# Kernel optimization log

Measured on AMD Instinct MI355X. Metric: run time of the kernel, lower is better.

## Reference

```python
import jax, jax.numpy as jnp
import numpy as np

K = 16        # num_p
SIGMA = 1.0
B, NA, NB, C = 2, 16384, 8192, 128
Z, Y, X = 64, 256, 256  # spatial_shape


def _unique_coords(rng, n):
    lin = rng.choice(Z * Y * X, size=n, replace=False)
    z = lin // (Y * X)
    y = (lin // X) % Y
    x = lin % X
    return np.stack([z, y, x], axis=-1).astype(np.float32)


def setup_inputs() -> dict:
    key = jax.random.key(0)
    k1, = jax.random.split(key, 1)
    rng = np.random.default_rng(0)
    # teacher voxel coords unique per batch -> bev_out_3d dedup is identity
    tpos = np.stack([_unique_coords(rng, NA) for _ in range(B)])          # [B, NA, 3]
    spos = np.stack([_unique_coords(rng, NB) for _ in range(B)])          # [B, NB, 3]
    tfeat = jax.random.normal(k1, (B, NA, C), dtype=jnp.float32)
    return {
        "teacher_features": tfeat,
        "teacher_positions": jnp.asarray(tpos),
        "student_positions": jnp.asarray(spos),
    }


def _knn_agg(feats, pa, pb):
    # feats: [NA, C], pa: [NA, 3] teacher coords, pb: [NB, 3] student coords
    # squared euclidean distances (same top-k ordering as cdist p=2)
    sq = (jnp.sum(pb * pb, -1, keepdims=True)
          - 2.0 * pb @ pa.T
          + jnp.sum(pa * pa, -1)[None, :])                                # [NB, NA]
    neg_sq_k, idx = jax.lax.top_k(-sq, K)                                 # smallest-k
    knn_sq = jnp.maximum(-neg_sq_k, 0.0)                                  # [NB, K] = knn_dist**2
    w = jnp.exp(-knn_sq / (2.0 * SIGMA ** 2))
    w = w / jnp.sum(w, axis=1, keepdims=True)
    knn_feats = feats[idx]                                                # [NB, K, C]
    return jnp.einsum('nkc,nk->nc', knn_feats, w)                         # [NB, C]


def reference(teacher_features, teacher_positions, student_positions):
    # per-batch knn_aggregation, batches have equal sizes -> vmap
    return jax.vmap(_knn_agg)(teacher_features, teacher_positions, student_positions)
```

## Files before the change

kernel.cpp:

```cpp
#include <hip/hip_runtime.h>
#include <math.h>
#include <stdint.h>

#define K_NN   16
#define BATCH  2
#define NA_    16384
#define NB_    8192
#define CH     128
#define CZ     4
#define CY     16
#define CX     16
#define NCELL  (CZ*CY*CX)
#define CSH    4
#define PADKEY 0xFFF00000u

#define OFF_META   65536
#define OFF_CURSOR 81920
#define OFF_SORTED 98304

__device__ __forceinline__ int cell_of(float p0, float p1, float p2) {
    const int cz = ((int)p0) >> CSH;
    const int cy = ((int)p1) >> CSH;
    const int cx = ((int)p2) >> CSH;
    return (cz * CY + cy) * CX + cx;
}


__global__ __launch_bounds__(256) void count_hist(const float* __restrict__ tpos,
                                                  int* __restrict__ partial) {
    __shared__ int h[NCELL];
    const int blk = blockIdx.x;
    const int t = threadIdx.x;
#pragma unroll
    for (int j = 0; j < NCELL / 256; ++j) h[t + j * 256] = 0;
    __syncthreads();
    const int base = blk * 2048;
#pragma unroll
    for (int i = 0; i < 8; ++i) {
        const float* p = tpos + (size_t)(base + i * 256 + t) * 3;
        atomicAdd(&h[cell_of(p[0], p[1], p[2])], 1);
    }
    __syncthreads();
#pragma unroll
    for (int j = 0; j < NCELL / 256; ++j) {
        const int c = t + j * 256;
        partial[blk * NCELL + c] = h[c];
    }
}


__global__ __launch_bounds__(1024) void scan_kernel(const int* __restrict__ partial,
                                                    int2* __restrict__ meta,
                                                    int* __restrict__ cursor) {
    __shared__ int wp[16];
    const int b = blockIdx.x, t = threadIdx.x, lane = t & 63, w = t >> 6;
    int c = 0;
#pragma unroll
    for (int k = 0; k < 8; ++k) c += partial[(b * 8 + k) * NCELL + t];
    int x = c;
#pragma unroll
    for (int off = 1; off < 64; off <<= 1) {
        int u = __shfl_up(x, off);
        if (lane >= off) x += u;
    }
    if (lane == 63) wp[w] = x;
    __syncthreads();
    if (t < 16) {
        int v = wp[t];
#pragma unroll
        for (int off = 1; off < 16; off <<= 1) {
            int u = __shfl_up(v, off);
            if (t >= off) v += u;
        }
        wp[t] = v;
    }
    __syncthreads();
    const int excl = x - c + (w ? wp[w - 1] : 0);
    meta[b * NCELL + t]   = make_int2(excl, c);
    cursor[b * NCELL + t] = excl;
}


__global__ __launch_bounds__(256) void scatter_kernel(const float* __restrict__ tpos,
                                                      int* __restrict__ cursor,
                                                      uint2* __restrict__ sorted) {
    const int i = blockIdx.x * 256 + threadIdx.x;
    const int b = i >> 14;
    const float* tp = tpos + (size_t)i * 3;
    const int pz = (int)tp[0], py = (int)tp[1], px = (int)tp[2];
    const int cell = ((pz >> CSH) * CY + (py >> CSH)) * CX + (px >> CSH);
    const int pos = atomicAdd(&cursor[b * NCELL + cell], 1);
    const uint32_t pk = ((uint32_t)pz << 16) | ((uint32_t)py << 8) | (uint32_t)px;
    sorted[(size_t)b * NA_ + pos] = make_uint2(pk, (uint32_t)(i & (NA_ - 1)));
}


template<int NS>
__device__ __forceinline__ void merge_extract(uint32_t (&k)[NS], uint32_t (&sel)[K_NN]) {
    uint32_t m = k[0];
#pragma unroll
    for (int j = 1; j < NS; ++j) m = min(m, k[j]);
#pragma unroll
    for (int r = 0; r < K_NN; ++r) {
        uint32_t v = m;
#pragma unroll
        for (int off = 32; off > 0; off >>= 1)
            v = min(v, (uint32_t)__shfl_xor((int)v, off));
        sel[r] = (uint32_t)__builtin_amdgcn_readfirstlane((int)v);
        if (m == v) {
#pragma unroll
            for (int j = 0; j < NS; ++j) k[j] = (k[j] == v) ? 0xFFFFFFFFu : k[j];
            m = k[0];
#pragma unroll
            for (int j = 1; j < NS; ++j) m = min(m, k[j]);
        }
    }
}

__device__ __forceinline__ uint32_t key_of(uint2 p, int sz, int sy, int sx) {
    const int pz = (int)(p.x >> 16);
    const int py = (int)((p.x >> 8) & 255u);
    const int px = (int)(p.x & 255u);
    const int dz = sz - pz, dy = sy - py, dx = sx - px;
    const uint32_t d2 = (uint32_t)(dz * dz + dy * dy + dx * dx);
    return (d2 << 14) | p.y;
}


__device__ __noinline__ void ring_fallback(int lane, int sz, int sy, int sx,
                                           int scz, int scy, int scx, int rcov,
                                           const int2* __restrict__ mb,
                                           const uint2* __restrict__ sb,
                                           uint32_t* selLds) {
    uint32_t sel[K_NN];
#pragma unroll
    for (int j = 0; j < K_NN; ++j) sel[j] = 0xFFFFFFFFu;

    for (int r = 1;; ++r) {
        uint32_t kl[K_NN];
#pragma unroll
        for (int j = 0; j < K_NN; ++j) kl[j] = PADKEY + 16 + j;
        if (r > 1) {
            uint32_t seed = 0xFFFFFFFFu;
#pragma unroll
            for (int j = 0; j < K_NN; ++j) if (lane == j) seed = sel[j];
            kl[0] = seed;
        }
        uint32_t curmax = kl[0];
#pragma unroll
        for (int j = 1; j < K_NN; ++j) curmax = max(curmax, kl[j]);

        for (int dz = -r; dz <= r; ++dz) {
            const int cz = scz + dz; if ((unsigned)cz >= CZ) continue;
            for (int dy = -r; dy <= r; ++dy) {
                const int cy = scy + dy; if ((unsigned)cy >= CY) continue;
                const int rowb = (cz * CY + cy) * CX;
                const bool fullrow = (r == 1) || (max(abs(dz), abs(dy)) == r);
                int xl[2], xh[2];
                if (fullrow) {
                    xl[0] = max(scx - r, 0); xh[0] = min(scx + r, CX - 1);
                    xl[1] = 1; xh[1] = 0;
                } else {
                    xl[0] = scx - r; xh[0] = scx - r;
                    xl[1] = scx + r; xh[1] = scx + r;
                    if (xl[0] < 0)      { xl[0] = 1; xh[0] = 0; }
                    if (xh[1] > CX - 1) { xl[1] = 1; xh[1] = 0; }
                }
#pragma unroll
                for (int q = 0; q < 2; ++q) {
                    if (xl[q] > xh[q]) continue;
                    const int2 mlo = mb[rowb + xl[q]];
                    const int2 mhi = mb[rowb + xh[q]];
                    const int st = mlo.x, ln = mhi.x + mhi.y - st;
                    for (int o = 0; o < ln; o += 64) {
                        const int j2 = o + lane;
                        const bool act = j2 < ln;
                        const uint2 p = sb[st + (act ? j2 : 0)];
                        uint32_t kv = key_of(p, sz, sy, sx);
                        kv = act ? kv : 0xFFFFFFFFu;
                        if (kv < curmax) {
#pragma unroll
                            for (int j = 0; j < K_NN; ++j)
                                kl[j] = (kl[j] == curmax) ? kv : kl[j];
                            curmax = kl[0];
#pragma unroll
                            for (int j = 1; j < K_NN; ++j) curmax = max(curmax, kl[j]);
                        }
                    }
                }
            }
        }
        merge_extract<K_NN>(kl, sel);
        const uint32_t d16 = sel[K_NN - 1] >> 14;
        if (d16 <= (uint32_t)(256 * r * r) || r >= rcov) break;
    }

    if (lane == 0) {
#pragma unroll
        for (int j = 0; j < K_NN; ++j) selLds[j] = sel[j];
    }
}


__global__ __launch_bounds__(256) void knn_cells_kernel(
    const float* __restrict__ tfeat,
    const float* __restrict__ spos,
    const int2*  __restrict__ meta,
    const uint2* __restrict__ sorted,
    float* __restrict__ out)
{
    __shared__ uint32_t sSel[4][16];

    const int tid  = threadIdx.x;
    const int lane = tid & 63;
    const int wave = tid >> 6;

    const int bpb = NB_ / 4;
    const int b = blockIdx.x / bpb;
    const int n = (blockIdx.x % bpb) * 4 + wave;

    const float* sp = spos + ((size_t)b * NB_ + n) * 3;
    const int sz = (int)sp[0], sy = (int)sp[1], sx = (int)sp[2];
    const int scz = __builtin_amdgcn_readfirstlane(sz >> CSH);
    const int scy = __builtin_amdgcn_readfirstlane(sy >> CSH);
    const int scx = __builtin_amdgcn_readfirstlane(sx >> CSH);

    int rcov = max(max(scx, CX - 1 - scx), max(scy, CY - 1 - scy));
    rcov = max(rcov, max(scz, CZ - 1 - scz));

    const int2*  mb = meta   + (size_t)b * NCELL;
    const uint2* sb = sorted + (size_t)b * NA_;

    int rstart[9], rlen[9];
    const int cxlo = max(scx - 1, 0), cxhi = min(scx + 1, CX - 1);
    int nov = 0; bool fast = true;
#pragma unroll
    for (int kk = 0; kk < 9; ++kk) {
        const int cz = scz + kk / 3 - 1, cy = scy + kk % 3 - 1;
        int st = 0, ln = 0;
        if ((unsigned)cz < CZ && (unsigned)cy < CY) {
            const int rowb = (cz * CY + cy) * CX;
            const int2 mlo = mb[rowb + cxlo];
            const int2 mhi = mb[rowb + cxhi];
            st = mlo.x; ln = mhi.x + mhi.y - mlo.x;
        }
        rstart[kk] = st; rlen[kk] = ln;
        if (ln > 64) ++nov;
        if (ln > 128) fast = false;
    }
    if (nov > 3) fast = false;

    int nselF = K_NN;
    bool done = false;

    if (fast) {
        uint32_t key[12];
#pragma unroll
        for (int j = 0; j < 12; ++j) key[j] = PADKEY + j;
        int oc = 9;
#pragma unroll
        for (int kk = 0; kk < 9; ++kk) {
            if (rlen[kk] > 0) {
                const bool act = lane < rlen[kk];
                const uint2 p = sb[rstart[kk] + (act ? lane : 0)];
                const uint32_t kv = key_of(p, sz, sy, sx);
                key[kk] = act ? kv : key[kk];
            }
            if (rlen[kk] > 64) {
                const int j2 = 64 + lane;
                const bool act = j2 < rlen[kk];
                const uint2 p = sb[rstart[kk] + (act ? j2 : 0)];
                const uint32_t kv = key_of(p, sz, sy, sx);
                if (oc == 9)       key[9]  = act ? kv : key[9];
                else if (oc == 10) key[10] = act ? kv : key[10];
                else               key[11] = act ? kv : key[11];
                ++oc;
            }
        }

        uint32_t kmin = key[0];
#pragma unroll
        for (int j = 1; j < 12; ++j) kmin = min(kmin, key[j]);
#pragma unroll
        for (int off = 32; off > 0; off >>= 1)
            kmin = min(kmin, (uint32_t)__shfl_xor((int)kmin, off));
        kmin = (uint32_t)__builtin_amdgcn_readfirstlane((int)kmin);
        const uint32_t dmin2 = kmin >> 14;

        if (dmin2 <= 264u) {
            const uint32_t keyT = (dmin2 + 25u) << 14;
            int nsel = 0;
#pragma unroll
            for (int j = 0; j < 12; ++j) {
                const bool pred = key[j] < keyT;
                const unsigned long long m = __ballot(pred);
                const int offp = __builtin_amdgcn_mbcnt_hi(
                    (uint32_t)(m >> 32), __builtin_amdgcn_mbcnt_lo((uint32_t)m, 0));
                const int dst = nsel + offp;
                if (pred && dst < K_NN) sSel[wave][dst] = key[j];
                nsel += (int)__builtin_popcountll(m);
            }
            if (nsel <= K_NN) {
                nselF = nsel;
                done = true;
            }
        }
    }

    if (!done)
        ring_fallback(lane, sz, sy, sx, scz, scy, scx, rcov, mb, sb, &sSel[wave][0]);
    __threadfence_block();

    const uint4 sA = *(const uint4*)&sSel[wave][0];
    const uint4 sB = *(const uint4*)&sSel[wave][4];
    const uint4 sC = *(const uint4*)&sSel[wave][8];
    const uint4 sD = *(const uint4*)&sSel[wave][12];
    uint32_t sel[K_NN];
    sel[0]  = (uint32_t)__builtin_amdgcn_readfirstlane((int)sA.x);
    sel[1]  = (uint32_t)__builtin_amdgcn_readfirstlane((int)sA.y);
    sel[2]  = (uint32_t)__builtin_amdgcn_readfirstlane((int)sA.z);
    sel[3]  = (uint32_t)__builtin_amdgcn_readfirstlane((int)sA.w);
    sel[4]  = (uint32_t)__builtin_amdgcn_readfirstlane((int)sB.x);
    sel[5]  = (uint32_t)__builtin_amdgcn_readfirstlane((int)sB.y);
    sel[6]  = (uint32_t)__builtin_amdgcn_readfirstlane((int)sB.z);
    sel[7]  = (uint32_t)__builtin_amdgcn_readfirstlane((int)sB.w);
    sel[8]  = (uint32_t)__builtin_amdgcn_readfirstlane((int)sC.x);
    sel[9]  = (uint32_t)__builtin_amdgcn_readfirstlane((int)sC.y);
    sel[10] = (uint32_t)__builtin_amdgcn_readfirstlane((int)sC.z);
    sel[11] = (uint32_t)__builtin_amdgcn_readfirstlane((int)sC.w);
    sel[12] = (uint32_t)__builtin_amdgcn_readfirstlane((int)sD.x);
    sel[13] = (uint32_t)__builtin_amdgcn_readfirstlane((int)sD.y);
    sel[14] = (uint32_t)__builtin_amdgcn_readfirstlane((int)sD.z);
    sel[15] = (uint32_t)__builtin_amdgcn_readfirstlane((int)sD.w);

    float w[K_NN];
    float wsum = 0.f;
#pragma unroll
    for (int j = 0; j < K_NN; ++j) w[j] = 0.f;
#pragma unroll
    for (int j = 0; j < 4; ++j) {
        if (j < nselF) { w[j] = __expf(-0.5f * (float)(sel[j] >> 14)); wsum += w[j]; }
    }
    if (nselF > 4) {
#pragma unroll
        for (int j = 4; j < 8; ++j) {
            if (j < nselF) { w[j] = __expf(-0.5f * (float)(sel[j] >> 14)); wsum += w[j]; }
        }
    }
    if (nselF > 8) {
#pragma unroll
        for (int j = 8; j < 12; ++j) {
            if (j < nselF) { w[j] = __expf(-0.5f * (float)(sel[j] >> 14)); wsum += w[j]; }
        }
    }
    if (nselF > 12) {
#pragma unroll
        for (int j = 12; j < 16; ++j) {
            if (j < nselF) { w[j] = __expf(-0.5f * (float)(sel[j] >> 14)); wsum += w[j]; }
        }
    }
    const float inv = 1.0f / wsum;

    const float* fb = tfeat + (size_t)b * NA_ * CH;
    float2 acc = make_float2(0.f, 0.f);
#pragma unroll
    for (int j = 0; j < 4; ++j) {
        if (j < nselF) {
            const float2 v = ((const float2*)(fb + (size_t)(sel[j] & 16383u) * CH))[lane];
            const float ww = w[j] * inv;
            acc.x += ww * v.x; acc.y += ww * v.y;
        }
    }
    if (nselF > 4) {
#pragma unroll
        for (int j = 4; j < 8; ++j) {
            if (j < nselF) {
                const float2 v = ((const float2*)(fb + (size_t)(sel[j] & 16383u) * CH))[lane];
                const float ww = w[j] * inv;
                acc.x += ww * v.x; acc.y += ww * v.y;
            }
        }
    }
    if (nselF > 8) {
#pragma unroll
        for (int j = 8; j < 12; ++j) {
            if (j < nselF) {
                const float2 v = ((const float2*)(fb + (size_t)(sel[j] & 16383u) * CH))[lane];
                const float ww = w[j] * inv;
                acc.x += ww * v.x; acc.y += ww * v.y;
            }
        }
    }
    if (nselF > 12) {
#pragma unroll
        for (int j = 12; j < 16; ++j) {
            if (j < nselF) {
                const float2 v = ((const float2*)(fb + (size_t)(sel[j] & 16383u) * CH))[lane];
                const float ww = w[j] * inv;
                acc.x += ww * v.x; acc.y += ww * v.y;
            }
        }
    }

    float2* o = (float2*)(out + ((size_t)b * NB_ + n) * CH);
    o[lane] = acc;
}


extern "C" void kernel_launch(void* const* d_in, const int* in_sizes, int n_in,
                              void* d_out, int out_size, void* d_ws, size_t ws_size,
                              hipStream_t stream) {
    const float* tfeat = (const float*)d_in[0];
    const float* tpos  = (const float*)d_in[1];
    const float* spos  = (const float*)d_in[2];
    float* out = (float*)d_out;

    char* ws = (char*)d_ws;
    int*   partial = (int*)(ws);
    int2*  meta    = (int2*)(ws + OFF_META);
    int*   cursor  = (int*)(ws + OFF_CURSOR);
    uint2* sorted  = (uint2*)(ws + OFF_SORTED);

    count_hist<<<16, 256, 0, stream>>>(tpos, partial);
    scan_kernel<<<BATCH, 1024, 0, stream>>>(partial, meta, cursor);
    scatter_kernel<<<(BATCH * NA_) / 256, 256, 0, stream>>>(tpos, cursor, sorted);
    knn_cells_kernel<<<BATCH * (NB_ / 4), 256, 0, stream>>>(tfeat, spos, meta, sorted, out);
}
```

Before: 41.77 us.

## Fuse scan and scatter into one kernel with per-chunk LDS cursors

Merges the prefix-scan and scatter kernels into a single 16-block kernel. Each block recomputes the per-batch cell scan, adds the counts of the preceding chunks from the partial histograms to get its own starting offsets, and scatters its 2048 points using shared-memory atomics instead of global atomics. This removes one kernel launch and the global cursor contention. In exchange the scatter runs on only 16 blocks and every block repeats the scan.

```diff
diff --git a/kernel.cpp b/kernel.cpp
--- a/kernel.cpp
+++ b/kernel.cpp
@@ -15,7 +15,6 @@
 #define PADKEY 0xFFF00000u
 
 #define OFF_META   65536
-#define OFF_CURSOR 81920
 #define OFF_SORTED 98304
 
 __device__ __forceinline__ int cell_of(float p0, float p1, float p2) {
@@ -49,15 +48,28 @@
 }
 
 
-__global__ __launch_bounds__(1024) void scan_kernel(const int* __restrict__ partial,
+__global__ __launch_bounds__(256) void scan_scatter(const float* __restrict__ tpos,
+                                                    const int* __restrict__ partial,
                                                     int2* __restrict__ meta,
-                                                    int* __restrict__ cursor) {
-    __shared__ int wp[16];
-    const int b = blockIdx.x, t = threadIdx.x, lane = t & 63, w = t >> 6;
-    int c = 0;
-#pragma unroll
-    for (int k = 0; k < 8; ++k) c += partial[(b * 8 + k) * NCELL + t];
-    int x = c;
+                                                    uint2* __restrict__ sorted) {
+    __shared__ int sCur[NCELL];
+    __shared__ int wp[4];
+
+    const int h = blockIdx.x;
+    const int b = h >> 3, hl = h & 7;
+    const int t = threadIdx.x;
+    const int lane = t & 63, w = t >> 6;
+
+    int tot0 = 0, tot1 = 0, tot2 = 0, tot3 = 0;
+    int pre0 = 0, pre1 = 0, pre2 = 0, pre3 = 0;
+#pragma unroll
+    for (int k = 0; k < 8; ++k) {
+        const int4 v = *(const int4*)(partial + (b * 8 + k) * NCELL + t * 4);
+        tot0 += v.x; tot1 += v.y; tot2 += v.z; tot3 += v.w;
+        if (k < hl) { pre0 += v.x; pre1 += v.y; pre2 += v.z; pre3 += v.w; }
+    }
+    const int tsum = tot0 + tot1 + tot2 + tot3;
+    int x = tsum;
 #pragma unroll
     for (int off = 1; off < 64; off <<= 1) {
         int u = __shfl_up(x, off);
@@ -65,33 +77,37 @@
     }
     if (lane == 63) wp[w] = x;
     __syncthreads();
-    if (t < 16) {
-        int v = wp[t];
-#pragma unroll
-        for (int off = 1; off < 16; off <<= 1) {
-            int u = __shfl_up(v, off);
-            if (t >= off) v += u;
-        }
-        wp[t] = v;
+    if (t == 0) {
+        int r = 0;
+#pragma unroll
+        for (int k = 0; k < 4; ++k) { const int v = wp[k]; wp[k] = r; r += v; }
     }
     __syncthreads();
-    const int excl = x - c + (w ? wp[w - 1] : 0);
-    meta[b * NCELL + t]   = make_int2(excl, c);
-    cursor[b * NCELL + t] = excl;
-}
-
-
-__global__ __launch_bounds__(256) void scatter_kernel(const float* __restrict__ tpos,
-                                                      int* __restrict__ cursor,
-                                                      uint2* __restrict__ sorted) {
-    const int i = blockIdx.x * 256 + threadIdx.x;
-    const int b = i >> 14;
-    const float* tp = tpos + (size_t)i * 3;
-    const int pz = (int)tp[0], py = (int)tp[1], px = (int)tp[2];
-    const int cell = ((pz >> CSH) * CY + (py >> CSH)) * CX + (px >> CSH);
-    const int pos = atomicAdd(&cursor[b * NCELL + cell], 1);
-    const uint32_t pk = ((uint32_t)pz << 16) | ((uint32_t)py << 8) | (uint32_t)px;
-    sorted[(size_t)b * NA_ + pos] = make_uint2(pk, (uint32_t)(i & (NA_ - 1)));
+    int e = x - tsum + wp[w];
+    const int c0 = t * 4;
+    if (hl == 0) {
+        meta[b * NCELL + c0 + 0] = make_int2(e, tot0);
+        meta[b * NCELL + c0 + 1] = make_int2(e + tot0, tot1);
+        meta[b * NCELL + c0 + 2] = make_int2(e + tot0 + tot1, tot2);
+        meta[b * NCELL + c0 + 3] = make_int2(e + tot0 + tot1 + tot2, tot3);
+    }
+    sCur[c0 + 0] = e + pre0;
+    sCur[c0 + 1] = e + tot0 + pre1;
+    sCur[c0 + 2] = e + tot0 + tot1 + pre2;
+    sCur[c0 + 3] = e + tot0 + tot1 + tot2 + pre3;
+    __syncthreads();
+
+    const float* tb = tpos + (size_t)(b * NA_ + hl * 2048) * 3;
+#pragma unroll
+    for (int i = 0; i < 8; ++i) {
+        const int pi = i * 256 + t;
+        const float* p = tb + (size_t)pi * 3;
+        const int pz = (int)p[0], py = (int)p[1], px = (int)p[2];
+        const int cell = ((pz >> CSH) * CY + (py >> CSH)) * CX + (px >> CSH);
+        const int pos = atomicAdd(&sCur[cell], 1);
+        const uint32_t pk = ((uint32_t)pz << 16) | ((uint32_t)py << 8) | (uint32_t)px;
+        sorted[(size_t)b * NA_ + pos] = make_uint2(pk, (uint32_t)(hl * 2048 + pi));
+    }
 }
 
 
@@ -418,11 +434,9 @@
     char* ws = (char*)d_ws;
     int*   partial = (int*)(ws);
     int2*  meta    = (int2*)(ws + OFF_META);
-    int*   cursor  = (int*)(ws + OFF_CURSOR);
     uint2* sorted  = (uint2*)(ws + OFF_SORTED);
 
     count_hist<<<16, 256, 0, stream>>>(tpos, partial);
-    scan_kernel<<<BATCH, 1024, 0, stream>>>(partial, meta, cursor);
-    scatter_kernel<<<(BATCH * NA_) / 256, 256, 0, stream>>>(tpos, cursor, sorted);
+    scan_scatter<<<16, 256, 0, stream>>>(tpos, partial, meta, sorted);
     knn_cells_kernel<<<BATCH * (NB_ / 4), 256, 0, stream>>>(tfeat, spos, meta, sorted, out);
 }
```

Measured after the change: 38.13 us. 1.1x faster.
